# Kernel tuning notes

Measured on AMD Instinct MI355X. Metric: run time of the kernel, lower is better.

The kernel has to match this reference:

```python
import jax, jax.numpy as jnp
import numpy as np

N_NODES = 50000
N_EDGES = 800000
IN, S1, S2, S3 = 64, 128, 64, 32


def _lin_init(key, fan_in, fan_out):
    kw, kb = jax.random.split(key)
    s = 1.0 / np.sqrt(fan_in)
    W = jax.random.uniform(kw, (fan_in, fan_out), minval=-s, maxval=s, dtype=jnp.float32)
    b = jax.random.uniform(kb, (fan_out,), minval=-s, maxval=s, dtype=jnp.float32)
    return W, b


def setup_inputs() -> dict:
    key = jax.random.key(0)
    ks = jax.random.split(key, 11)
    x = jax.random.normal(ks[0], (N_NODES, IN), dtype=jnp.float32)
    src = jax.random.randint(ks[1], (N_EDGES,), 0, N_NODES)
    dst = jax.random.randint(ks[2], (N_EDGES,), 0, N_NODES)
    W_n1, b_n1 = _lin_init(ks[3], IN, S1)
    W_c1, b_c1 = _lin_init(ks[4], S1, S2)
    W_n2, b_n2 = _lin_init(ks[5], S1, S2)
    W_c2, b_c2 = _lin_init(ks[6], S2, S3)
    W_n3, b_n3 = _lin_init(ks[7], S2, S3)
    W_c3, b_c3 = _lin_init(ks[8], S3, 1)
    W_g1, b_g1 = _lin_init(ks[9], S2, S3)
    W_g2, b_g2 = _lin_init(ks[10], S3, 1)
    return {
        'pre_node_embedding': x, 'src': src, 'dst': dst,
        'W_n1': W_n1, 'b_n1': b_n1, 'W_c1': W_c1, 'b_c1': b_c1,
        'W_n2': W_n2, 'b_n2': b_n2, 'W_c2': W_c2, 'b_c2': b_c2,
        'W_n3': W_n3, 'b_n3': b_n3, 'W_c3': W_c3, 'b_c3': b_c3,
        'W_g1': W_g1, 'b_g1': b_g1, 'W_g2': W_g2, 'b_g2': b_g2,
    }


def _node_update(W, b, emb, src, dst, n_nodes):
    # gather neighbor states along edges, scatter-add onto destinations
    agg = jax.ops.segment_sum(emb[src], dst, num_segments=n_nodes)  # [N, d_in]
    return jax.nn.sigmoid((emb + agg) @ W + b)                      # [N, d_out]


def _conduit_update(W, b, emb, src, dst):
    # conduit (edge) embedding from its two endpoint nodes
    return jax.nn.sigmoid((emb[src] + emb[dst]) @ W + b)            # [E, d_out]


def reference(pre_node_embedding, src, dst,
              W_n1, b_n1, W_c1, b_c1, W_n2, b_n2, W_c2, b_c2,
              W_n3, b_n3, W_c3, b_c3, W_g1, b_g1, W_g2, b_g2):
    n = pre_node_embedding.shape[0]
    h1 = _node_update(W_n1, b_n1, pre_node_embedding, src, dst, n)  # [N, S1]
    c1 = _conduit_update(W_c1, b_c1, h1, src, dst)                  # [E, S2]
    h2 = _node_update(W_n2, b_n2, h1, src, dst, n)                  # [N, S2]
    c2 = _conduit_update(W_c2, b_c2, h2, src, dst)                  # [E, S3]
    g1 = jax.nn.sigmoid(c1 @ W_g1 + b_g1 + c2)                      # [E, S3]
    h3 = _node_update(W_n3, b_n3, h2, src, dst, n)                  # [N, S3]
    c3 = _conduit_update(W_c3, b_c3, h3, src, dst)                  # [E, 1]
    out = jax.nn.sigmoid(g1 @ W_g2 + b_g2 + c3)                     # [E, 1]
    return out
```

## Files before the change

kernel.cpp:

```cpp
#include <hip/hip_runtime.h>

#define N_NODES 50000
#define N_EDGES 800000
#define CVT_B 6250
#define NODE_B ((N_NODES + 63) / 64)
#define EDGE_B (N_EDGES / 128)
#define NB 196
#define FILL_B 196
#define FILL_CHUNK 4096

typedef _Float16 h2 __attribute__((ext_vector_type(2)));
typedef _Float16 f16x8 __attribute__((ext_vector_type(8)));
typedef float f32x4 __attribute__((ext_vector_type(4)));

__device__ __forceinline__ float sigf(float v) {
  return __builtin_amdgcn_rcpf(1.0f + __expf(-v));
}
__device__ __forceinline__ unsigned packh2(float a, float b) {
  return __builtin_bit_cast(unsigned, __builtin_amdgcn_cvt_pkrtz(a, b));
}
__device__ __forceinline__ float2 unpackh2(unsigned u) {
  h2 p = __builtin_bit_cast(h2, u);
  return make_float2((float)p.x, (float)p.y);
}
__device__ __forceinline__ void acc8(float* a, uint4 v) {
  float2 p0 = unpackh2(v.x), p1 = unpackh2(v.y);
  float2 p2 = unpackh2(v.z), p3 = unpackh2(v.w);
  a[0] += p0.x; a[1] += p0.y; a[2] += p1.x; a[3] += p1.y;
  a[4] += p2.x; a[5] += p2.y; a[6] += p3.x; a[7] += p3.y;
}
__device__ __forceinline__ unsigned addpk(unsigned a, unsigned b) {
  h2 r = __builtin_bit_cast(h2, a) + __builtin_bit_cast(h2, b);
  return __builtin_bit_cast(unsigned, r);
}
#define MFMA16(A, B, C) __builtin_amdgcn_mfma_f32_16x16x32_f16(A, __builtin_bit_cast(f16x8, B), C, 0, 0, 0)

__global__ __launch_bounds__(256) void prep_kernel(
    const float* __restrict__ x, unsigned* __restrict__ x16,
    const int* __restrict__ dst, int* __restrict__ histM,
    const float* __restrict__ Wn1, const float* __restrict__ Wn2,
    const float* __restrict__ Wc1, const float* __restrict__ Wn3,
    const float* __restrict__ Wc2, const float* __restrict__ Wg1,
    uint4* __restrict__ Wn1f, uint4* __restrict__ Wn2f, uint4* __restrict__ Wc1f,
    uint4* __restrict__ Wn3f, uint4* __restrict__ Wc2f, uint4* __restrict__ Wg1f)
{
  int b = blockIdx.x;
  if (b < CVT_B) {
    int i = b * 256 + threadIdx.x;
    float2 v = ((const float2*)x)[i];
    x16[i] = packh2(v.x, v.y);
  } else if (b < CVT_B + FILL_B) {
    __shared__ int hist[NB];
    int tid = threadIdx.x, bid = b - CVT_B;
    if (tid < NB) hist[tid] = 0;
    __syncthreads();
    int ebase = bid * FILL_CHUNK;
#pragma unroll
    for (int it = 0; it < FILL_CHUNK / 256; ++it) {
      int e = ebase + it * 256 + tid;
      if (e < N_EDGES) atomicAdd(&hist[dst[e] >> 8], 1);
    }
    __syncthreads();
    if (tid < NB) histM[bid * NB + tid] = hist[tid];
  } else {
    int lane = threadIdx.x & 63, w = threadIdx.x >> 6;
    int n15 = lane & 15, chunk = lane >> 4;
    if (w == 0) {
#pragma unroll
      for (int f = 0; f < 16; ++f) {
        int nt = f >> 1, ks = f & 1;
        int n = nt * 16 + n15;
        f16x8 vv;
#pragma unroll
        for (int i = 0; i < 8; ++i) vv[i] = (_Float16)Wn1[(ks * 32 + chunk * 8 + i) * 128 + n];
        Wn1f[f * 64 + lane] = __builtin_bit_cast(uint4, vv);
      }
    } else if (w == 1) {
#pragma unroll
      for (int f = 0; f < 16; ++f) {
        int nt = f >> 2, ks = f & 3;
        int n = nt * 16 + n15;
        f16x8 vv;
#pragma unroll
        for (int i = 0; i < 8; ++i) vv[i] = (_Float16)Wn2[(ks * 32 + chunk * 8 + i) * 64 + n];
        Wn2f[f * 64 + lane] = __builtin_bit_cast(uint4, vv);
      }
    } else if (w == 2) {
#pragma unroll
      for (int f = 0; f < 16; ++f) {
        int nt = f >> 2, ks = f & 3;
        int n = nt * 16 + n15;
        f16x8 vv;
#pragma unroll
        for (int i = 0; i < 8; ++i) vv[i] = (_Float16)Wc1[(ks * 32 + chunk * 8 + i) * 64 + n];
        Wc1f[f * 64 + lane] = __builtin_bit_cast(uint4, vv);
      }
    } else {
#pragma unroll
      for (int f = 0; f < 4; ++f) {
        int nt = f >> 1, ks = f & 1;
        int n = nt * 16 + n15;
        f16x8 v3, vc;
#pragma unroll
        for (int i = 0; i < 8; ++i) {
          int k = ks * 32 + chunk * 8 + i;
          v3[i] = (_Float16)Wn3[k * 32 + n];
          vc[i] = (_Float16)Wc2[k * 32 + n];
        }
        Wn3f[f * 64 + lane] = __builtin_bit_cast(uint4, v3);
        Wc2f[f * 64 + lane] = __builtin_bit_cast(uint4, vc);
      }
#pragma unroll
      for (int ks = 0; ks < 2; ++ks)
#pragma unroll
        for (int nh = 0; nh < 2; ++nh) {
          f16x8 vv;
#pragma unroll
          for (int i = 0; i < 8; ++i)
            vv[i] = (_Float16)Wg1[(ks * 32 + chunk * 8 + i) * 32 + nh * 16 + n15];
          Wg1f[(ks * 2 + nh) * 64 + lane] = __builtin_bit_cast(uint4, vv);
        }
    }
  }
}

__global__ __launch_bounds__(256) void scanA_kernel(
    const int* __restrict__ histM, int* __restrict__ colOff,
    int* __restrict__ bucketBase)
{
  int j = threadIdx.x, lane = j & 63, w = j >> 6;
  int total = 0;
  if (j < NB)
    for (int i = 0; i < FILL_B; ++i) total += histM[i * NB + j];
  int x = total;
#pragma unroll
  for (int off = 1; off < 64; off <<= 1) {
    int y = __shfl_up(x, off);
    if (lane >= off) x += y;
  }
  __shared__ int ws[4];
  if (lane == 63) ws[w] = x;
  __syncthreads();
  int woff = 0;
#pragma unroll
  for (int k = 0; k < 4; ++k) if (k < w) woff += ws[k];
  int excl = woff + x - total;
  if (j < NB) {
    bucketBase[j] = excl;
    int running = excl;
    for (int i = 0; i < FILL_B; ++i) {
      colOff[i * NB + j] = running;
      running += histM[i * NB + j];
    }
    if (j == NB - 1) bucketBase[NB] = running;
  }
}

__global__ __launch_bounds__(256) void fill2_kernel(
    const int* __restrict__ src, const int* __restrict__ dst,
    const int* __restrict__ colOff, uint2* __restrict__ cem)
{
  __shared__ int cur[NB];
  int tid = threadIdx.x, bid = blockIdx.x;
  if (tid < NB) cur[tid] = colOff[bid * NB + tid];
  __syncthreads();
  int ebase = bid * FILL_CHUNK;
#pragma unroll
  for (int it = 0; it < FILL_CHUNK / 256; ++it) {
    int e = ebase + it * 256 + tid;
    if (e < N_EDGES) {
      int s = src[e], d = dst[e];
      int pos = atomicAdd(&cur[d >> 8], 1);
      cem[pos] = make_uint2((unsigned)s, ((unsigned)(d & 255) << 20) | (unsigned)e);
    }
  }
}

__global__ __launch_bounds__(256) void fill3_kernel(
    const uint2* __restrict__ cem, const int* __restrict__ bucketBase,
    uint2* __restrict__ ce, unsigned short* __restrict__ col16,
    int* __restrict__ rowptr)
{
  __shared__ int cnt[256], curs[256], ws[4];
  int j = blockIdx.x, tid = threadIdx.x;
  int base = bucketBase[j], endb = bucketBase[j + 1];
  cnt[tid] = 0;
  __syncthreads();
  for (int k = base + tid; k < endb; k += 256)
    atomicAdd(&cnt[(cem[k].y >> 20) & 255], 1);
  __syncthreads();
  int v = cnt[tid];
  int lane = tid & 63, w = tid >> 6;
  int x = v;
#pragma unroll
  for (int off = 1; off < 64; off <<= 1) {
    int y = __shfl_up(x, off);
    if (lane >= off) x += y;
  }
  if (lane == 63) ws[w] = x;
  __syncthreads();
  int woff = 0;
#pragma unroll
  for (int k = 0; k < 4; ++k) if (k < w) woff += ws[k];
  int ex = woff + x - v;
  curs[tid] = ex;
  int n = j * 256 + tid;
  if (n < N_NODES) {
    rowptr[n + 1] = base + ex + v;
    if (n == 0) rowptr[0] = 0;
  }
  __syncthreads();
  for (int k = base + tid; k < endb; k += 256) {
    uint2 r = cem[k];
    int dlow = (r.y >> 20) & 255;
    int pos = base + atomicAdd(&curs[dlow], 1);
    unsigned d = (unsigned)(j * 256 + dlow);
    ce[pos] = make_uint2(r.x | (d << 16), r.y & 0xFFFFFu);
    col16[pos] = (unsigned short)r.x;
  }
}

__global__ __launch_bounds__(256) void gather1_kernel(
    const unsigned* __restrict__ X16, const int* __restrict__ rowptr,
    const unsigned short* __restrict__ col16, unsigned* __restrict__ T16)
{
  int w = threadIdx.x >> 6, lane = threadIdx.x & 63;
  int n = blockIdx.x * 4 + w;
  if (n >= N_NODES) return;
  int beg = rowptr[n], end = rowptr[n + 1];
  int q = lane >> 3, c = lane & 7;
  const uint4* feat4 = (const uint4*)X16;
  float a[8] = {0.f, 0.f, 0.f, 0.f, 0.f, 0.f, 0.f, 0.f};
  for (int k0 = beg; k0 < end; k0 += 64) {
    int kk = k0 + lane;
    int cv = (kk < end) ? (int)col16[kk] : 0;
    int m = end - k0; if (m > 64) m = 64;
    int e = 0;
#pragma unroll 2
    for (; e + 7 < m; e += 8) {
      int se = __shfl(cv, e + q);
      acc8(a, feat4[(size_t)se * 8 + c]);
    }
    int r = m - e;
    if (r) {
      int idx = e + q; if (idx >= m) idx = m - 1;
      int se = __shfl(cv, idx);
      uint4 v = feat4[(size_t)se * 8 + c];
      if (q < r) acc8(a, v);
    }
  }
#pragma unroll
  for (int j = 0; j < 8; ++j) {
    a[j] += __shfl_xor(a[j], 32);
    a[j] += __shfl_xor(a[j], 16);
    a[j] += __shfl_xor(a[j], 8);
  }
  if (q == 0) {
    uint4 xv = ((const uint4*)X16)[(size_t)n * 8 + c];
    float2 x0 = unpackh2(xv.x), x1 = unpackh2(xv.y);
    float2 x2 = unpackh2(xv.z), x3 = unpackh2(xv.w);
    uint4 o;
    o.x = packh2(a[0] + x0.x, a[1] + x0.y);
    o.y = packh2(a[2] + x1.x, a[3] + x1.y);
    o.z = packh2(a[4] + x2.x, a[5] + x2.y);
    o.w = packh2(a[6] + x3.x, a[7] + x3.y);
    ((uint4*)T16)[(size_t)n * 8 + c] = o;
  }
}

__global__ __launch_bounds__(256) void gather2_kernel(
    const unsigned* __restrict__ Q2u, const int* __restrict__ rowptr,
    const unsigned short* __restrict__ col16, const float* __restrict__ bn2,
    unsigned* __restrict__ H2)
{
  int w = threadIdx.x >> 6, lane = threadIdx.x & 63;
  int n = blockIdx.x * 4 + w;
  if (n >= N_NODES) return;
  int beg = rowptr[n], end = rowptr[n + 1];
  int q = lane >> 3, c = lane & 7;
  const uint4* feat4 = (const uint4*)Q2u;
  float a[8] = {0.f, 0.f, 0.f, 0.f, 0.f, 0.f, 0.f, 0.f};
  for (int k0 = beg; k0 < end; k0 += 64) {
    int kk = k0 + lane;
    int cv = (kk < end) ? (int)col16[kk] : 0;
    int m = end - k0; if (m > 64) m = 64;
    int e = 0;
#pragma unroll 2
    for (; e + 7 < m; e += 8) {
      int se = __shfl(cv, e + q);
      acc8(a, feat4[(size_t)se * 8 + c]);
    }
    int r = m - e;
    if (r) {
      int idx = e + q; if (idx >= m) idx = m - 1;
      int se = __shfl(cv, idx);
      uint4 v = feat4[(size_t)se * 8 + c];
      if (q < r) acc8(a, v);
    }
  }
#pragma unroll
  for (int j = 0; j < 8; ++j) {
    a[j] += __shfl_xor(a[j], 32);
    a[j] += __shfl_xor(a[j], 16);
    a[j] += __shfl_xor(a[j], 8);
  }
  if (q == 0) {
    uint4 qv = ((const uint4*)Q2u)[(size_t)n * 8 + c];
    float4 bnA = ((const float4*)bn2)[2 * c];
    float4 bnB = ((const float4*)bn2)[2 * c + 1];
    float2 q0 = unpackh2(qv.x), q1 = unpackh2(qv.y);
    float2 q2 = unpackh2(qv.z), q3 = unpackh2(qv.w);
    uint4 o;
    o.x = packh2(sigf(a[0] + q0.x + bnA.x), sigf(a[1] + q0.y + bnA.y));
    o.y = packh2(sigf(a[2] + q1.x + bnA.z), sigf(a[3] + q1.y + bnA.w));
    o.z = packh2(sigf(a[4] + q2.x + bnB.x), sigf(a[5] + q2.y + bnB.y));
    o.w = packh2(sigf(a[6] + q3.x + bnB.z), sigf(a[7] + q3.y + bnB.w));
    ((uint4*)H2)[(size_t)n * 8 + c] = o;
  }
}

__global__ __launch_bounds__(256) void gather3_kernel(
    const unsigned* __restrict__ Q3u, const int* __restrict__ rowptr,
    const unsigned short* __restrict__ col16, const float* __restrict__ bn3,
    const float* __restrict__ Wc3, _Float16* __restrict__ P3h)
{
  int w = threadIdx.x >> 6, lane = threadIdx.x & 63;
  int n = blockIdx.x * 4 + w;
  if (n >= N_NODES) return;
  int beg = rowptr[n], end = rowptr[n + 1];
  int q = lane >> 2, c = lane & 3;
  const uint4* feat4 = (const uint4*)Q3u;
  float a[8] = {0.f, 0.f, 0.f, 0.f, 0.f, 0.f, 0.f, 0.f};
  for (int k0 = beg; k0 < end; k0 += 64) {
    int kk = k0 + lane;
    int cv = (kk < end) ? (int)col16[kk] : 0;
    int m = end - k0; if (m > 64) m = 64;
    int e = 0;
#pragma unroll 2
    for (; e + 15 < m; e += 16) {
      int se = __shfl(cv, e + q);
      acc8(a, feat4[(size_t)se * 4 + c]);
    }
    int r = m - e;
    if (r) {
      int idx = e + q; if (idx >= m) idx = m - 1;
      int se = __shfl(cv, idx);
      uint4 v = feat4[(size_t)se * 4 + c];
      if (q < r) acc8(a, v);
    }
  }
#pragma unroll
  for (int j = 0; j < 8; ++j) {
    a[j] += __shfl_xor(a[j], 32);
    a[j] += __shfl_xor(a[j], 16);
    a[j] += __shfl_xor(a[j], 8);
    a[j] += __shfl_xor(a[j], 4);
  }
  if (q == 0) {
    uint4 qv = feat4[(size_t)n * 4 + c];
    float4 bnA = ((const float4*)bn3)[2 * c], bnB = ((const float4*)bn3)[2 * c + 1];
    float4 wcA = ((const float4*)Wc3)[2 * c], wcB = ((const float4*)Wc3)[2 * c + 1];
    float2 q0 = unpackh2(qv.x), q1 = unpackh2(qv.y);
    float2 q2 = unpackh2(qv.z), q3 = unpackh2(qv.w);
    float p = sigf(a[0] + q0.x + bnA.x) * wcA.x + sigf(a[1] + q0.y + bnA.y) * wcA.y
            + sigf(a[2] + q1.x + bnA.z) * wcA.z + sigf(a[3] + q1.y + bnA.w) * wcA.w
            + sigf(a[4] + q2.x + bnB.x) * wcB.x + sigf(a[5] + q2.y + bnB.y) * wcB.y
            + sigf(a[6] + q3.x + bnB.z) * wcB.z + sigf(a[7] + q3.y + bnB.w) * wcB.w;
    p += __shfl_xor(p, 1); p += __shfl_xor(p, 2);
    if (c == 0) P3h[n] = (_Float16)p;
  }
}

__global__ __launch_bounds__(256) void node1_kernel(
    const unsigned* __restrict__ T16,
    const uint4* __restrict__ Wn1f, const uint4* __restrict__ Wn2f,
    const uint4* __restrict__ Wc1f, const float* __restrict__ bn1,
    _Float16* __restrict__ Q2h, _Float16* __restrict__ P1h)
{
  __shared__ __align__(16) _Float16 t_lds[64 * 72];
  __shared__ __align__(16) _Float16 h1_lds[64 * 136];
  int tid = threadIdx.x;
  int lane = tid & 63, w = tid >> 6;
  int nbase = blockIdx.x * 64;

#pragma unroll
  for (int rep = 0; rep < 2; ++rep) {
    int uidx = rep * 1024 + tid * 4;
    int node = uidx >> 5, c = uidx & 31;
    int gn = nbase + node; if (gn > N_NODES - 1) gn = N_NODES - 1;
    uint4 tv = *(const uint4*)(T16 + (size_t)gn * 32 + c);
    *(uint4*)(t_lds + node * 72 + c * 2) = tv;
  }
  __syncthreads();

  int row16 = lane & 15, chunk = lane >> 4;
  uint4 b1[2][2];
#pragma unroll
  for (int ntl = 0; ntl < 2; ++ntl)
#pragma unroll
    for (int ks = 0; ks < 2; ++ks)
      b1[ntl][ks] = Wn1f[((2 * w + ntl) * 2 + ks) * 64 + lane];

  f32x4 acc[4][2];
#pragma unroll
  for (int mt = 0; mt < 4; ++mt)
#pragma unroll
    for (int ntl = 0; ntl < 2; ++ntl) acc[mt][ntl] = (f32x4){0.f, 0.f, 0.f, 0.f};
#pragma unroll
  for (int mt = 0; mt < 4; ++mt) {
    const _Float16* ab = t_lds + (mt * 16 + row16) * 72 + chunk * 8;
    f16x8 A0 = *(const f16x8*)ab;
    f16x8 A1 = *(const f16x8*)(ab + 32);
#pragma unroll
    for (int ntl = 0; ntl < 2; ++ntl) {
      acc[mt][ntl] = MFMA16(A0, b1[ntl][0], acc[mt][ntl]);
      acc[mt][ntl] = MFMA16(A1, b1[ntl][1], acc[mt][ntl]);
    }
  }
  float bnv0 = bn1[w * 32 + row16], bnv1 = bn1[w * 32 + 16 + row16];
#pragma unroll
  for (int mt = 0; mt < 4; ++mt)
#pragma unroll
    for (int r = 0; r < 4; ++r) {
      int rowl = mt * 16 + chunk * 4 + r;
      h1_lds[rowl * 136 + w * 32 + row16]      = (_Float16)sigf(acc[mt][0][r] + bnv0);
      h1_lds[rowl * 136 + w * 32 + 16 + row16] = (_Float16)sigf(acc[mt][1][r] + bnv1);
    }
  __syncthreads();

#pragma unroll
  for (int job = 0; job < 2; ++job) {
    const uint4* Wf = job ? Wc1f : Wn2f;
    uint4 bf[4];
#pragma unroll
    for (int ks = 0; ks < 4; ++ks) bf[ks] = Wf[(w * 4 + ks) * 64 + lane];
    f32x4 a2[4];
#pragma unroll
    for (int mt = 0; mt < 4; ++mt) a2[mt] = (f32x4){0.f, 0.f, 0.f, 0.f};
#pragma unroll
    for (int mt = 0; mt < 4; ++mt) {
      const _Float16* hb = h1_lds + (mt * 16 + row16) * 136 + chunk * 8;
#pragma unroll
      for (int ks = 0; ks < 4; ++ks) {
        f16x8 A = *(const f16x8*)(hb + ks * 32);
        a2[mt] = MFMA16(A, bf[ks], a2[mt]);
      }
    }
    _Float16* op = job ? P1h : Q2h;
#pragma unroll
    for (int mt = 0; mt < 4; ++mt)
#pragma unroll
      for (int r = 0; r < 4; ++r) {
        int gn = nbase + mt * 16 + chunk * 4 + r;
        if (gn < N_NODES) op[(size_t)gn * 64 + w * 16 + row16] = (_Float16)a2[mt][r];
      }
  }
}

__global__ __launch_bounds__(256) void node2_kernel(
    const unsigned* __restrict__ H2,
    const uint4* __restrict__ Wn3f, const uint4* __restrict__ Wc2f,
    _Float16* __restrict__ Q3h, _Float16* __restrict__ P2h)
{
  __shared__ __align__(16) _Float16 t_lds[64 * 72];
  int tid = threadIdx.x, lane = tid & 63, w = tid >> 6;
  int nbase = blockIdx.x * 64;
#pragma unroll
  for (int rep = 0; rep < 2; ++rep) {
    int uidx = rep * 1024 + tid * 4;
    int node = uidx >> 5, c = uidx & 31;
    int gn = nbase + node; if (gn > N_NODES - 1) gn = N_NODES - 1;
    uint4 tv = *(const uint4*)(H2 + (size_t)gn * 32 + c);
    *(uint4*)(t_lds + node * 72 + c * 2) = tv;
  }
  __syncthreads();
  int row16 = lane & 15, chunk = lane >> 4;
  int mat = w >> 1, nt = w & 1;
  const uint4* Wf = mat ? Wc2f : Wn3f;
  uint4 bf0 = Wf[(nt * 2 + 0) * 64 + lane];
  uint4 bf1 = Wf[(nt * 2 + 1) * 64 + lane];
  f32x4 a2[4];
#pragma unroll
  for (int mt = 0; mt < 4; ++mt) a2[mt] = (f32x4){0.f, 0.f, 0.f, 0.f};
#pragma unroll
  for (int mt = 0; mt < 4; ++mt) {
    const _Float16* ab = t_lds + (mt * 16 + row16) * 72 + chunk * 8;
    f16x8 A0 = *(const f16x8*)ab;
    f16x8 A1 = *(const f16x8*)(ab + 32);
    a2[mt] = MFMA16(A0, bf0, a2[mt]);
    a2[mt] = MFMA16(A1, bf1, a2[mt]);
  }
  _Float16* op = mat ? P2h : Q3h;
#pragma unroll
  for (int mt = 0; mt < 4; ++mt)
#pragma unroll
    for (int r = 0; r < 4; ++r) {
      int gn = nbase + mt * 16 + chunk * 4 + r;
      if (gn < N_NODES) op[(size_t)gn * 32 + nt * 16 + row16] = (_Float16)a2[mt][r];
    }
}

__global__ __launch_bounds__(256) void edge_kernel(
    const uint2* __restrict__ ce,
    const unsigned* __restrict__ P1_16, const unsigned* __restrict__ P2_16,
    const _Float16* __restrict__ P3_16, const uint4* __restrict__ Bfrag,
    const float* __restrict__ bc1, const float* __restrict__ bc2,
    const float* __restrict__ bc3, const float* __restrict__ bg1,
    const float* __restrict__ Wg2, const float* __restrict__ bg2,
    float* __restrict__ out)
{
  __shared__ __align__(16) _Float16 sbuf[4][32 * 104];
  __shared__ int eidx[4][64];
  __shared__ int eido[4][32];
  int lane = threadIdx.x & 63;
  int w = threadIdx.x >> 6;
  int b = blockIdx.x;
  int xcd = b & 7, idx = b >> 3;
  int swz = (xcd < 2 ? xcd * 782 : 2 * 782 + (xcd - 2) * 781) + idx;
  int ebase = swz * 128 + w * 32;
  _Float16* wb = &sbuf[w][0];

  int e32 = lane & 31;
  uint2 cv2 = ce[ebase + e32];
  int sv = (int)(cv2.x & 0xFFFFu);
  int dv = (int)(cv2.x >> 16);
  int myi = (lane < 32) ? sv : dv;
  eidx[w][lane] = myi;
  if (lane < 32) eido[w][e32] = (int)cv2.y;

  f16x8 Bf[2][2];
#pragma unroll
  for (int ks = 0; ks < 2; ++ks)
#pragma unroll
    for (int nh = 0; nh < 2; ++nh)
      Bf[ks][nh] = __builtin_bit_cast(f16x8, Bfrag[(ks * 2 + nh) * 64 + lane]);

  {
    float p3v = (float)P3_16[myi];
    float pair = __shfl_xor(p3v, 32);
    if (lane < 32) wb[e32 * 104 + 96] = (_Float16)(p3v + pair);
  }
  {
    int c = lane & 7, q = lane >> 3;
    unsigned b10 = packh2(bc1[8 * c],     bc1[8 * c + 1]);
    unsigned b11 = packh2(bc1[8 * c + 2], bc1[8 * c + 3]);
    unsigned b12 = packh2(bc1[8 * c + 4], bc1[8 * c + 5]);
    unsigned b13 = packh2(bc1[8 * c + 6], bc1[8 * c + 7]);
#pragma unroll
    for (int it = 0; it < 4; ++it) {
      int e = 8 * it + q;
      int s = eidx[w][e];
      int d = eidx[w][32 + e];
      uint4 ps = *(const uint4*)(P1_16 + (size_t)s * 32 + 4 * c);
      uint4 pd = *(const uint4*)(P1_16 + (size_t)d * 32 + 4 * c);
      h2 v0 = __builtin_bit_cast(h2, addpk(addpk(ps.x, pd.x), b10));
      h2 v1 = __builtin_bit_cast(h2, addpk(addpk(ps.y, pd.y), b11));
      h2 v2 = __builtin_bit_cast(h2, addpk(addpk(ps.z, pd.z), b12));
      h2 v3 = __builtin_bit_cast(h2, addpk(addpk(ps.w, pd.w), b13));
      uint4 o;
      o.x = packh2(sigf((float)v0.x), sigf((float)v0.y));
      o.y = packh2(sigf((float)v1.x), sigf((float)v1.y));
      o.z = packh2(sigf((float)v2.x), sigf((float)v2.y));
      o.w = packh2(sigf((float)v3.x), sigf((float)v3.y));
      *(uint4*)(wb + e * 104 + 8 * c) = o;
    }
  }
  {
    int c = lane & 3, q = lane >> 2;
    unsigned b20 = packh2(bc2[8 * c],     bc2[8 * c + 1]);
    unsigned b21 = packh2(bc2[8 * c + 2], bc2[8 * c + 3]);
    unsigned b22 = packh2(bc2[8 * c + 4], bc2[8 * c + 5]);
    unsigned b23 = packh2(bc2[8 * c + 6], bc2[8 * c + 7]);
#pragma unroll
    for (int it = 0; it < 2; ++it) {
      int e = 16 * it + q;
      int s = eidx[w][e];
      int d = eidx[w][32 + e];
      uint4 ps = *(const uint4*)(P2_16 + (size_t)s * 16 + 4 * c);
      uint4 pd = *(const uint4*)(P2_16 + (size_t)d * 16 + 4 * c);
      h2 v0 = __builtin_bit_cast(h2, addpk(addpk(ps.x, pd.x), b20));
      h2 v1 = __builtin_bit_cast(h2, addpk(addpk(ps.y, pd.y), b21));
      h2 v2 = __builtin_bit_cast(h2, addpk(addpk(ps.z, pd.z), b22));
      h2 v3 = __builtin_bit_cast(h2, addpk(addpk(ps.w, pd.w), b23));
      uint4 o;
      o.x = packh2(sigf((float)v0.x), sigf((float)v0.y));
      o.y = packh2(sigf((float)v1.x), sigf((float)v1.y));
      o.z = packh2(sigf((float)v2.x), sigf((float)v2.y));
      o.w = packh2(sigf((float)v3.x), sigf((float)v3.y));
      *(uint4*)(wb + e * 104 + 64 + 8 * c) = o;
    }
  }

  int row = lane & 15, chunk = lane >> 4;
  float bg1v0 = bg1[row], bg1v1 = bg1[16 + row];
  float wg2v0 = Wg2[row], wg2v1 = Wg2[16 + row];
  float bg2v = bg2[0], bc3v = bc3[0];
#pragma unroll
  for (int g = 0; g < 2; ++g) {
    const _Float16* abase = wb + (16 * g + row) * 104 + chunk * 8;
    f16x8 A0 = *(const f16x8*)abase;
    f16x8 A1 = *(const f16x8*)(abase + 32);
    f32x4 acc0 = {0.f, 0.f, 0.f, 0.f}, acc1 = {0.f, 0.f, 0.f, 0.f};
    acc0 = __builtin_amdgcn_mfma_f32_16x16x32_f16(A0, Bf[0][0], acc0, 0, 0, 0);
    acc1 = __builtin_amdgcn_mfma_f32_16x16x32_f16(A0, Bf[0][1], acc1, 0, 0, 0);
    acc0 = __builtin_amdgcn_mfma_f32_16x16x32_f16(A1, Bf[1][0], acc0, 0, 0, 0);
    acc1 = __builtin_amdgcn_mfma_f32_16x16x32_f16(A1, Bf[1][1], acc1, 0, 0, 0);
#pragma unroll
    for (int r = 0; r < 4; ++r) {
      int e = 16 * g + chunk * 4 + r;
      float c2a = (float)wb[e * 104 + 64 + row];
      float c2b = (float)wb[e * 104 + 80 + row];
      float v0 = sigf(acc0[r] + bg1v0 + c2a) * wg2v0;
      float v1 = sigf(acc1[r] + bg1v1 + c2b) * wg2v1;
      float part = v0 + v1;
      part += __shfl_xor(part, 1);
      part += __shfl_xor(part, 2);
      part += __shfl_xor(part, 4);
      part += __shfl_xor(part, 8);
      float c3v = (float)wb[e * 104 + 96];
      if (row == 0)
        out[eido[w][e]] = sigf(part + bg2v + sigf(c3v + bc3v));
    }
  }
}

extern "C" void kernel_launch(void* const* d_in, const int* in_sizes, int n_in,
                              void* d_out, int out_size, void* d_ws, size_t ws_size,
                              hipStream_t stream)
{
  const float* x   = (const float*)d_in[0];
  const int*   src = (const int*)d_in[1];
  const int*   dst = (const int*)d_in[2];
  const float* Wn1 = (const float*)d_in[3];
  const float* bn1 = (const float*)d_in[4];
  const float* Wc1 = (const float*)d_in[5];
  const float* bc1 = (const float*)d_in[6];
  const float* Wn2 = (const float*)d_in[7];
  const float* bn2 = (const float*)d_in[8];
  const float* Wc2 = (const float*)d_in[9];
  const float* bc2 = (const float*)d_in[10];
  const float* Wn3 = (const float*)d_in[11];
  const float* bn3 = (const float*)d_in[12];
  const float* Wc3 = (const float*)d_in[13];
  const float* bc3 = (const float*)d_in[14];
  const float* Wg1 = (const float*)d_in[15];
  const float* bg1 = (const float*)d_in[16];
  const float* Wg2 = (const float*)d_in[17];
  const float* bg2 = (const float*)d_in[18];
  float* out = (float*)d_out;

  char* base = (char*)d_ws;
  unsigned* TMP16 = (unsigned*)base; base += (size_t)N_NODES * 32 * 4;
  unsigned* X16   = (unsigned*)base; base += (size_t)N_NODES * 32 * 4;
  unsigned* Q2_16 = (unsigned*)base; base += (size_t)N_NODES * 32 * 4;
  unsigned* P1_16 = (unsigned*)base; base += (size_t)N_NODES * 32 * 4;
  unsigned* Q3_16 = (unsigned*)base; base += (size_t)N_NODES * 16 * 4;
  unsigned* P2_16 = (unsigned*)base; base += (size_t)N_NODES * 16 * 4;
  _Float16* P3_16 = (_Float16*)base; base += ((size_t)N_NODES * 2 + 15) / 16 * 16;
  int* rowptr = (int*)base;          base += (size_t)(N_NODES + 1) * 4 + 12;
  uint2* ce   = (uint2*)base;        base += (size_t)N_EDGES * 8;
  uint2* cem  = (uint2*)base;        base += (size_t)N_EDGES * 8;
  unsigned short* col16 = (unsigned short*)base; base += ((size_t)N_EDGES * 2 + 15) / 16 * 16;
  int* histM  = (int*)base;          base += (size_t)FILL_B * NB * 4;
  int* colOff = (int*)base;          base += (size_t)FILL_B * NB * 4;
  int* bucketBase = (int*)base;      base += (size_t)(NB + 1) * 4 + 12;
  uint4* Wg1f = (uint4*)base;        base += 4 * 64 * 16;
  uint4* Wn1f = (uint4*)base;        base += 16 * 64 * 16;
  uint4* Wn2f = (uint4*)base;        base += 16 * 64 * 16;
  uint4* Wc1f = (uint4*)base;        base += 16 * 64 * 16;
  uint4* Wn3f = (uint4*)base;        base += 4 * 64 * 16;
  uint4* Wc2f = (uint4*)base;        base += 4 * 64 * 16;

  prep_kernel<<<CVT_B + FILL_B + 1, 256, 0, stream>>>(x, X16, dst, histM,
      Wn1, Wn2, Wc1, Wn3, Wc2, Wg1, Wn1f, Wn2f, Wc1f, Wn3f, Wc2f, Wg1f);
  scanA_kernel<<<1, 256, 0, stream>>>(histM, colOff, bucketBase);
  fill2_kernel<<<FILL_B, 256, 0, stream>>>(src, dst, colOff, cem);
  fill3_kernel<<<NB, 256, 0, stream>>>(cem, bucketBase, ce, col16, rowptr);

  gather1_kernel<<<(N_NODES + 3) / 4, 256, 0, stream>>>(X16, rowptr, col16, TMP16);
  node1_kernel<<<NODE_B, 256, 0, stream>>>(TMP16, Wn1f, Wn2f, Wc1f, bn1,
      (_Float16*)Q2_16, (_Float16*)P1_16);
  gather2_kernel<<<(N_NODES + 3) / 4, 256, 0, stream>>>(Q2_16, rowptr, col16, bn2, TMP16);
  node2_kernel<<<NODE_B, 256, 0, stream>>>(TMP16, Wn3f, Wc2f,
      (_Float16*)Q3_16, (_Float16*)P2_16);
  gather3_kernel<<<(N_NODES + 3) / 4, 256, 0, stream>>>(Q3_16, rowptr, col16, bn3, Wc3, P3_16);
  edge_kernel<<<EDGE_B, 256, 0, stream>>>(ce, P1_16, P2_16, P3_16, Wg1f,
      bc1, bc2, bc3, bg1, Wg2, bg2, out);
}
```

Before: 178.0 us.

## Parallelize histogram scan across blocks and shrink edge kernel blocks

The single-block serial column scan over the fill histogram is split into a per-column parallel scan kernel (one block per bucket) plus a small scan of column totals. fill2 now adds the bucket base to each column offset. The edge kernel is also relaunched with 128-thread blocks (two wavefronts) and twice as many blocks, with the XCD swizzle updated to match. This trades one extra launch for removing a serial 196-iteration loop, and makes the edge-kernel scheduling finer-grained.

Result: faster. 172.0 us (-3.4%).

```diff
diff --git a/kernel.cpp b/kernel.cpp
--- a/kernel.cpp
+++ b/kernel.cpp
@@ -4,7 +4,7 @@
 #define N_EDGES 800000
 #define CVT_B 6250
 #define NODE_B ((N_NODES + 63) / 64)
-#define EDGE_B (N_EDGES / 128)
+#define EDGE_B2 (N_EDGES / 64)
 #define NB 196
 #define FILL_B 196
 #define FILL_CHUNK 4096
@@ -124,15 +124,15 @@
   }
 }
 
-__global__ __launch_bounds__(256) void scanA_kernel(
+__global__ __launch_bounds__(256) void scanA1_kernel(
     const int* __restrict__ histM, int* __restrict__ colOff,
-    int* __restrict__ bucketBase)
-{
-  int j = threadIdx.x, lane = j & 63, w = j >> 6;
-  int total = 0;
-  if (j < NB)
-    for (int i = 0; i < FILL_B; ++i) total += histM[i * NB + j];
-  int x = total;
+    int* __restrict__ colTot)
+{
+  int j = blockIdx.x;
+  int i = threadIdx.x;
+  int lane = i & 63, w = i >> 6;
+  int v = (i < FILL_B) ? histM[i * NB + j] : 0;
+  int x = v;
 #pragma unroll
   for (int off = 1; off < 64; off <<= 1) {
     int y = __shfl_up(x, off);
@@ -144,25 +144,41 @@
   int woff = 0;
 #pragma unroll
   for (int k = 0; k < 4; ++k) if (k < w) woff += ws[k];
-  int excl = woff + x - total;
-  if (j < NB) {
-    bucketBase[j] = excl;
-    int running = excl;
-    for (int i = 0; i < FILL_B; ++i) {
-      colOff[i * NB + j] = running;
-      running += histM[i * NB + j];
-    }
-    if (j == NB - 1) bucketBase[NB] = running;
-  }
+  int excl = woff + x - v;
+  if (i < FILL_B) colOff[i * NB + j] = excl;
+  if (i == FILL_B - 1) colTot[j] = excl + v;
+}
+
+__global__ __launch_bounds__(256) void scanA2_kernel(
+    const int* __restrict__ colTot, int* __restrict__ bucketBase)
+{
+  int j = threadIdx.x, lane = j & 63, w = j >> 6;
+  int v = (j < NB) ? colTot[j] : 0;
+  int x = v;
+#pragma unroll
+  for (int off = 1; off < 64; off <<= 1) {
+    int y = __shfl_up(x, off);
+    if (lane >= off) x += y;
+  }
+  __shared__ int ws[4];
+  if (lane == 63) ws[w] = x;
+  __syncthreads();
+  int woff = 0;
+#pragma unroll
+  for (int k = 0; k < 4; ++k) if (k < w) woff += ws[k];
+  int excl = woff + x - v;
+  if (j < NB) bucketBase[j] = excl;
+  if (j == NB - 1) bucketBase[NB] = excl + v;
 }
 
 __global__ __launch_bounds__(256) void fill2_kernel(
     const int* __restrict__ src, const int* __restrict__ dst,
-    const int* __restrict__ colOff, uint2* __restrict__ cem)
+    const int* __restrict__ colOff, const int* __restrict__ bucketBase,
+    uint2* __restrict__ cem)
 {
   __shared__ int cur[NB];
   int tid = threadIdx.x, bid = blockIdx.x;
-  if (tid < NB) cur[tid] = colOff[bid * NB + tid];
+  if (tid < NB) cur[tid] = colOff[bid * NB + tid] + bucketBase[tid];
   __syncthreads();
   int ebase = bid * FILL_CHUNK;
 #pragma unroll
@@ -500,7 +516,7 @@
     }
 }
 
-__global__ __launch_bounds__(256) void edge_kernel(
+__global__ __launch_bounds__(128) void edge_kernel(
     const uint2* __restrict__ ce,
     const unsigned* __restrict__ P1_16, const unsigned* __restrict__ P2_16,
     const _Float16* __restrict__ P3_16, const uint4* __restrict__ Bfrag,
@@ -509,15 +525,15 @@
     const float* __restrict__ Wg2, const float* __restrict__ bg2,
     float* __restrict__ out)
 {
-  __shared__ __align__(16) _Float16 sbuf[4][32 * 104];
-  __shared__ int eidx[4][64];
-  __shared__ int eido[4][32];
+  __shared__ __align__(16) _Float16 sbuf[2][32 * 104];
+  __shared__ int eidx[2][64];
+  __shared__ int eido[2][32];
   int lane = threadIdx.x & 63;
   int w = threadIdx.x >> 6;
   int b = blockIdx.x;
   int xcd = b & 7, idx = b >> 3;
-  int swz = (xcd < 2 ? xcd * 782 : 2 * 782 + (xcd - 2) * 781) + idx;
-  int ebase = swz * 128 + w * 32;
+  int swz = (xcd < 4 ? xcd * 1563 : 4 * 1563 + (xcd - 4) * 1562) + idx;
+  int ebase = swz * 64 + w * 32;
   _Float16* wb = &sbuf[w][0];
 
   int e32 = lane & 31;
@@ -663,6 +679,7 @@
   unsigned short* col16 = (unsigned short*)base; base += ((size_t)N_EDGES * 2 + 15) / 16 * 16;
   int* histM  = (int*)base;          base += (size_t)FILL_B * NB * 4;
   int* colOff = (int*)base;          base += (size_t)FILL_B * NB * 4;
+  int* colTot = (int*)base;          base += (size_t)NB * 4;
   int* bucketBase = (int*)base;      base += (size_t)(NB + 1) * 4 + 12;
   uint4* Wg1f = (uint4*)base;        base += 4 * 64 * 16;
   uint4* Wn1f = (uint4*)base;        base += 16 * 64 * 16;
@@ -673,8 +690,9 @@
 
   prep_kernel<<<CVT_B + FILL_B + 1, 256, 0, stream>>>(x, X16, dst, histM,
       Wn1, Wn2, Wc1, Wn3, Wc2, Wg1, Wn1f, Wn2f, Wc1f, Wn3f, Wc2f, Wg1f);
-  scanA_kernel<<<1, 256, 0, stream>>>(histM, colOff, bucketBase);
-  fill2_kernel<<<FILL_B, 256, 0, stream>>>(src, dst, colOff, cem);
+  scanA1_kernel<<<NB, 256, 0, stream>>>(histM, colOff, colTot);
+  scanA2_kernel<<<1, 256, 0, stream>>>(colTot, bucketBase);
+  fill2_kernel<<<FILL_B, 256, 0, stream>>>(src, dst, colOff, bucketBase, cem);
   fill3_kernel<<<NB, 256, 0, stream>>>(cem, bucketBase, ce, col16, rowptr);
 
   gather1_kernel<<<(N_NODES + 3) / 4, 256, 0, stream>>>(X16, rowptr, col16, TMP16);
@@ -684,6 +702,6 @@
   node2_kernel<<<NODE_B, 256, 0, stream>>>(TMP16, Wn3f, Wc2f,
       (_Float16*)Q3_16, (_Float16*)P2_16);
   gather3_kernel<<<(N_NODES + 3) / 4, 256, 0, stream>>>(Q3_16, rowptr, col16, bn3, Wc3, P3_16);
-  edge_kernel<<<EDGE_B, 256, 0, stream>>>(ce, P1_16, P2_16, P3_16, Wg1f,
+  edge_kernel<<<EDGE_B2, 128, 0, stream>>>(ce, P1_16, P2_16, P3_16, Wg1f,
       bc1, bc2, bc3, bg1, Wg2, bg2, out);
 }
```
